# Optimization experiments

Hardware: AMD Instinct MI355X
Metric: run time of the kernel (lower is better)

## Reference

```python
import jax, jax.numpy as jnp
import numpy as np

B, N, NFEAT, NHID, NOUT, NMLP, NCLASS = 32, 1024, 128, 64, 64, 128, 2
ALPHA = 0.2  # leaky relu slope
NEG = -9e15


def setup_inputs() -> dict:
    key = jax.random.key(0)
    ks = jax.random.split(key, 12)
    x = jax.random.normal(ks[0], (B, N, NFEAT), dtype=jnp.float32)
    x_mask = (jax.random.uniform(ks[1], (B, N)) < 0.9).astype(jnp.float32)
    adj = (jax.random.uniform(ks[2], (B, N, N)) < 0.05).astype(jnp.float32)
    adj = jnp.maximum(adj, jnp.eye(N, dtype=jnp.float32)[None])  # self loops
    s = 0.02
    W0 = jax.random.normal(ks[3], (NFEAT, NHID), dtype=jnp.float32) * s
    a0 = jax.random.normal(ks[4], (2 * NHID, 1), dtype=jnp.float32) * s
    Wout = jax.random.normal(ks[5], (NHID, NOUT), dtype=jnp.float32) * s
    aout = jax.random.normal(ks[6], (2 * NOUT, 1), dtype=jnp.float32) * s
    W1 = jax.random.normal(ks[7], (NOUT, NMLP), dtype=jnp.float32) * s
    b1 = jnp.zeros((NMLP,), dtype=jnp.float32)
    W2 = jax.random.normal(ks[8], (NMLP, NCLASS), dtype=jnp.float32) * s
    b2 = jnp.zeros((NCLASS,), dtype=jnp.float32)
    return {"x": x, "x_mask": x_mask, "adj": adj, "W0": W0, "a0": a0,
            "Wout": Wout, "aout": aout, "W1": W1, "b1": b1, "W2": W2, "b2": b2}


def _gat_layer(h, adj, W, a):
    # h: [B,N,F_in], W: [F_in,F_out], a: [2*F_out,1]
    Wh = jnp.einsum('bnf,fh->bnh', h, W)                 # [B,N,F_out]
    d = W.shape[1]
    f1 = Wh @ a[:d]                                      # [B,N,1]
    f2 = Wh @ a[d:]                                      # [B,N,1]
    e = jax.nn.leaky_relu(f1 + jnp.swapaxes(f2, 1, 2), ALPHA)  # [B,N,N]
    e = jnp.where(adj > 0, e, NEG)
    attn = jax.nn.softmax(e, axis=-1)
    return jnp.einsum('bnm,bmh->bnh', attn, Wh)


def reference(x, x_mask, adj, W0, a0, Wout, aout, W1, b1, W2, b2):
    # Only head 0 reaches out_att in the original (zip truncation); dropout is
    # identity in eval mode.
    h = jax.nn.elu(_gat_layer(x, adj, W0, a0))           # concat=True -> elu
    h = jax.nn.elu(_gat_layer(h, adj, Wout, aout))       # F.elu applied outside
    m = x_mask[..., None]
    g = jnp.sum(h * m, axis=1) / jnp.maximum(jnp.sum(x_mask, axis=1, keepdims=True), 1.0)  # masked mean readout [B,NOUT]
    return jax.nn.relu(g @ W1 + b1) @ W2 + b2            # [B,NCLASS]
```

## Files before the change

kernel.cpp:

```cpp
#include <hip/hip_runtime.h>
#include <math.h>

#define BB 32
#define NN 1024
#define NFEAT 128
#define ALPHA 0.2f
#define MAXD 128

#define WH1_TILE_BLOCKS (BB * NN / 64)
#define ATTN_BLOCKS (BB * NN / 4)

template<int FIN>
__device__ __forceinline__ void wh_tile_body(
    const int blk, const int tid,
    const float* __restrict__ hin, const float* __restrict__ W,
    const float* __restrict__ a, float* __restrict__ Wh,
    float* __restrict__ f1, float* __restrict__ f2) {
  const int tx = tid & 15;
  const int ty = tid >> 4;
  const int row0 = blk * 64 + ty * 4;

  float4 acc[4];
#pragma unroll
  for (int i = 0; i < 4; ++i) acc[i] = make_float4(0.f, 0.f, 0.f, 0.f);

#pragma unroll 4
  for (int k = 0; k < FIN; k += 4) {
    float4 wv[4];
#pragma unroll
    for (int i = 0; i < 4; ++i)
      wv[i] = *reinterpret_cast<const float4*>(&W[(size_t)(k + i) * 64 + tx * 4]);
#pragma unroll
    for (int i = 0; i < 4; ++i) {
      const float4 xv = *reinterpret_cast<const float4*>(
          &hin[(size_t)(row0 + i) * FIN + k]);
      acc[i].x = fmaf(xv.x, wv[0].x, acc[i].x);
      acc[i].y = fmaf(xv.x, wv[0].y, acc[i].y);
      acc[i].z = fmaf(xv.x, wv[0].z, acc[i].z);
      acc[i].w = fmaf(xv.x, wv[0].w, acc[i].w);
      acc[i].x = fmaf(xv.y, wv[1].x, acc[i].x);
      acc[i].y = fmaf(xv.y, wv[1].y, acc[i].y);
      acc[i].z = fmaf(xv.y, wv[1].z, acc[i].z);
      acc[i].w = fmaf(xv.y, wv[1].w, acc[i].w);
      acc[i].x = fmaf(xv.z, wv[2].x, acc[i].x);
      acc[i].y = fmaf(xv.z, wv[2].y, acc[i].y);
      acc[i].z = fmaf(xv.z, wv[2].z, acc[i].z);
      acc[i].w = fmaf(xv.z, wv[2].w, acc[i].w);
      acc[i].x = fmaf(xv.w, wv[3].x, acc[i].x);
      acc[i].y = fmaf(xv.w, wv[3].y, acc[i].y);
      acc[i].z = fmaf(xv.w, wv[3].z, acc[i].z);
      acc[i].w = fmaf(xv.w, wv[3].w, acc[i].w);
    }
  }

  const float4 av1 = *reinterpret_cast<const float4*>(&a[tx * 4]);
  const float4 av2 = *reinterpret_cast<const float4*>(&a[64 + tx * 4]);
#pragma unroll
  for (int i = 0; i < 4; ++i) {
    const int row = row0 + i;
    *reinterpret_cast<float4*>(&Wh[(size_t)row * 64 + tx * 4]) = acc[i];
    float c1 = acc[i].x * av1.x + acc[i].y * av1.y + acc[i].z * av1.z + acc[i].w * av1.w;
    float c2 = acc[i].x * av2.x + acc[i].y * av2.y + acc[i].z * av2.z + acc[i].w * av2.w;
#pragma unroll
    for (int off = 8; off > 0; off >>= 1) {
      c1 += __shfl_xor(c1, off, 64);
      c2 += __shfl_xor(c2, off, 64);
    }
    if (tx == 0) { f1[row] = c1; f2[row] = c2; }
  }
}

__global__ __launch_bounds__(256) void wh1_kernel(
    const float* __restrict__ x, const float* __restrict__ W0,
    const float* __restrict__ a0, float* __restrict__ Wh,
    float* __restrict__ f1, float* __restrict__ f2) {
  wh_tile_body<NFEAT>(blockIdx.x, threadIdx.x, x, W0, a0, Wh, f1, f2);
}

__global__ __launch_bounds__(256) void nbr_build_kernel(
    const float* __restrict__ adj, unsigned short* __restrict__ nbr,
    int* __restrict__ cnt) {
  __shared__ unsigned short stageW[4][128];
  __shared__ unsigned short merged[MAXD];
  __shared__ int cnts[4];
  const int row = blockIdx.x;
  const int wv = threadIdx.x >> 6, lane = threadIdx.x & 63;
  const float* adjrow = adj + (size_t)row * NN;

  const float4 av = *reinterpret_cast<const float4*>(&adjrow[wv * 256 + lane * 4]);
  if (threadIdx.x < 64)
    reinterpret_cast<unsigned int*>(merged)[threadIdx.x] = 0u;

  const unsigned long long lmask = (1ull << lane) - 1ull;
  const int m = (av.x > 0.f ? 1 : 0) | (av.y > 0.f ? 2 : 0) |
                (av.z > 0.f ? 4 : 0) | (av.w > 0.f ? 8 : 0);
  const unsigned long long b0 = __ballot(m & 1);
  const unsigned long long b1 = __ballot(m & 2);
  const unsigned long long b2 = __ballot(m & 4);
  const unsigned long long b3 = __ballot(m & 8);
  int base = __popcll(b0 & lmask) + __popcll(b1 & lmask) +
             __popcll(b2 & lmask) + __popcll(b3 & lmask);
  const int e0 = wv * 256 + lane * 4;
  if (m & 1) { if (base < 128) stageW[wv][base] = (unsigned short)(e0);     ++base; }
  if (m & 2) { if (base < 128) stageW[wv][base] = (unsigned short)(e0 + 1); ++base; }
  if (m & 4) { if (base < 128) stageW[wv][base] = (unsigned short)(e0 + 2); ++base; }
  if (m & 8) { if (base < 128) stageW[wv][base] = (unsigned short)(e0 + 3); ++base; }
  if (lane == 0)
    cnts[wv] = __popcll(b0) + __popcll(b1) + __popcll(b2) + __popcll(b3);
  __syncthreads();
  const int c0 = cnts[0], c1 = cnts[1], c2 = cnts[2], c3 = cnts[3];
  const int off = (wv == 0) ? 0 : (wv == 1) ? c0 : (wv == 2) ? c0 + c1 : c0 + c1 + c2;
  const int cw  = (wv == 0) ? c0 : (wv == 1) ? c1 : (wv == 2) ? c2 : c3;
  if (lane < cw && off + lane < MAXD) merged[off + lane] = stageW[wv][lane];
  if (64 + lane < cw && off + 64 + lane < MAXD)
    merged[off + 64 + lane] = stageW[wv][64 + lane];
  __syncthreads();
  if (threadIdx.x < 64)
    reinterpret_cast<unsigned int*>(nbr + (size_t)row * MAXD)[threadIdx.x] =
        reinterpret_cast<const unsigned int*>(merged)[threadIdx.x];
  if (threadIdx.x == 0) {
    const int total = c0 + c1 + c2 + c3;
    cnt[row] = total < MAXD ? total : MAXD;
  }
}

__device__ __forceinline__ void attn_softmax(
    const unsigned short* __restrict__ nrow, const int count,
    const float f1n, const float* __restrict__ f2b,
    float* ps, unsigned short* msh, const int lane) {
  int m0 = 0, m1 = 0;
  const bool on0 = lane < count, on1 = 64 + lane < count;
  float e0 = -3e38f, e1 = -3e38f;
  if (on0) { m0 = nrow[lane];      float v = f1n + f2b[m0]; e0 = v > 0.f ? v : ALPHA * v; }
  if (on1) { m1 = nrow[64 + lane]; float v = f1n + f2b[m1]; e1 = v > 0.f ? v : ALPHA * v; }
  float lmax = fmaxf(e0, e1);
#pragma unroll
  for (int off = 32; off > 0; off >>= 1) lmax = fmaxf(lmax, __shfl_xor(lmax, off, 64));
  float p0 = on0 ? __expf(e0 - lmax) : 0.f;
  float p1 = on1 ? __expf(e1 - lmax) : 0.f;
  float ls = p0 + p1;
#pragma unroll
  for (int off = 32; off > 0; off >>= 1) ls += __shfl_xor(ls, off, 64);
  const float inv = 1.f / ls;
  ps[lane] = p0 * inv;  ps[64 + lane] = p1 * inv;
  msh[lane] = (unsigned short)m0;  msh[64 + lane] = (unsigned short)m1;
}

__device__ __forceinline__ float attn_gather(
    const float* ps, const unsigned short* msh, const int count,
    const float* __restrict__ Whb, const int lane) {
  float a0 = 0.f, a1 = 0.f, a2 = 0.f, a3 = 0.f;
  float a4 = 0.f, a5 = 0.f, a6 = 0.f, a7 = 0.f;
  const int c8 = count & ~7;
  int k = 0;
  for (; k < c8; k += 8) {
    const float4  pa = *reinterpret_cast<const float4*>(&ps[k]);
    const float4  pb = *reinterpret_cast<const float4*>(&ps[k + 4]);
    const ushort4 ia = *reinterpret_cast<const ushort4*>(&msh[k]);
    const ushort4 ib = *reinterpret_cast<const ushort4*>(&msh[k + 4]);
    a0 = fmaf(pa.x, Whb[(size_t)ia.x * 64 + lane], a0);
    a1 = fmaf(pa.y, Whb[(size_t)ia.y * 64 + lane], a1);
    a2 = fmaf(pa.z, Whb[(size_t)ia.z * 64 + lane], a2);
    a3 = fmaf(pa.w, Whb[(size_t)ia.w * 64 + lane], a3);
    a4 = fmaf(pb.x, Whb[(size_t)ib.x * 64 + lane], a4);
    a5 = fmaf(pb.y, Whb[(size_t)ib.y * 64 + lane], a5);
    a6 = fmaf(pb.z, Whb[(size_t)ib.z * 64 + lane], a6);
    a7 = fmaf(pb.w, Whb[(size_t)ib.w * 64 + lane], a7);
  }
  for (; k < count; ++k)
    a0 = fmaf(ps[k], Whb[(size_t)msh[k] * 64 + lane], a0);
  return ((a0 + a1) + (a2 + a3)) + ((a4 + a5) + (a6 + a7));
}

__global__ __launch_bounds__(256) void attn1_kernel(
    const unsigned short* __restrict__ nbr, const int* __restrict__ cnt,
    const float* __restrict__ f1, const float* __restrict__ f2,
    const float* __restrict__ Wh,
    const float* __restrict__ Wnext, const float* __restrict__ anext,
    float* __restrict__ WhOut, float* __restrict__ f1o,
    float* __restrict__ f2o) {
  __shared__ float ps[4][MAXD];
  __shared__ unsigned short msh[4][MAXD];
  __shared__ float h1s[4][64];
  const int wv = threadIdx.x >> 6, lane = threadIdx.x & 63;
  const int j = blockIdx.x;
  const int batch = (j & 7) + 8 * (j >> 11);
  const int chunk = (j >> 3) & 255;
  const int row = (batch * 256 + chunk) * 4 + wv;

  int count = cnt[row];
  if (count > MAXD) count = MAXD;
  attn_softmax(nbr + (size_t)row * MAXD, count, f1[row],
               f2 + (size_t)batch * NN, ps[wv], msh[wv], lane);
  const float acc = attn_gather(ps[wv], msh[wv], count,
                                Wh + (size_t)batch * (NN * 64), lane);
  const float hval = acc > 0.f ? acc : expm1f(acc);

  h1s[wv][lane] = hval;
  float s = 0.f;
#pragma unroll 8
  for (int f = 0; f < 64; ++f)
    s = fmaf(h1s[wv][f], Wnext[f * 64 + lane], s);
  WhOut[(size_t)row * 64 + lane] = s;
  float c1 = s * anext[lane];
  float c2 = s * anext[64 + lane];
#pragma unroll
  for (int off = 32; off > 0; off >>= 1) {
    c1 += __shfl_xor(c1, off, 64);
    c2 += __shfl_xor(c2, off, 64);
  }
  if (lane == 0) { f1o[row] = c1; f2o[row] = c2; }
}

__global__ __launch_bounds__(256) void attn2_kernel(
    const unsigned short* __restrict__ nbr, const int* __restrict__ cnt,
    const float* __restrict__ f1, const float* __restrict__ f2,
    const float* __restrict__ Wh, const float* __restrict__ mask,
    float* __restrict__ part2) {
  __shared__ float ps[4][MAXD];
  __shared__ unsigned short msh[4][MAXD];
  __shared__ float agg[4][64];
  const int wv = threadIdx.x >> 6, lane = threadIdx.x & 63;
  const int j = blockIdx.x;
  const int batch = (j & 7) + 8 * (j >> 11);
  const int chunk = (j >> 3) & 255;
  const int row = (batch * 256 + chunk) * 4 + wv;

  int count = cnt[row];
  if (count > MAXD) count = MAXD;
  attn_softmax(nbr + (size_t)row * MAXD, count, f1[row],
               f2 + (size_t)batch * NN, ps[wv], msh[wv], lane);
  const float acc = attn_gather(ps[wv], msh[wv], count,
                                Wh + (size_t)batch * (NN * 64), lane);
  const float hval = acc > 0.f ? acc : expm1f(acc);

  const float mv = mask[row];
  agg[wv][lane] = mv * hval;
  __syncthreads();
  if (wv == 0)
    part2[(size_t)(batch * 256 + chunk) * 64 + lane] =
        (agg[0][lane] + agg[1][lane]) + (agg[2][lane] + agg[3][lane]);
}

__global__ __launch_bounds__(256) void mlp2_kernel(
    const float* __restrict__ part2, const float* __restrict__ mask,
    const float* __restrict__ W1, const float* __restrict__ b1,
    const float* __restrict__ W2, const float* __restrict__ b2,
    float* __restrict__ outp) {
  const int b = blockIdx.x;
  const int tid = threadIdx.x;
  const int wv = tid >> 6, lane = tid & 63;
  __shared__ float aggG[4][64];
  __shared__ float msW[4];
  __shared__ float g[64];
  __shared__ float hid[128];

  const float4 mv4 = *reinterpret_cast<const float4*>(&mask[(size_t)b * NN + tid * 4]);
  float ms = (mv4.x + mv4.y) + (mv4.z + mv4.w);
#pragma unroll
  for (int off = 32; off > 0; off >>= 1) ms += __shfl_xor(ms, off, 64);
  if (lane == 0) msW[wv] = ms;

  float gs = 0.f;
  const float* pb = part2 + ((size_t)b * 256 + wv * 64) * 64 + lane;
#pragma unroll 8
  for (int i = 0; i < 64; ++i) gs += pb[(size_t)i * 64];
  aggG[wv][lane] = gs;
  __syncthreads();
  const float denom = fmaxf((msW[0] + msW[1]) + (msW[2] + msW[3]), 1.0f);
  if (tid < 64)
    g[tid] = ((aggG[0][tid] + aggG[1][tid]) + (aggG[2][tid] + aggG[3][tid])) / denom;
  __syncthreads();
  if (tid < 128) {
    float s = b1[tid];
#pragma unroll 8
    for (int k = 0; k < 64; ++k) s += g[k] * W1[k * 128 + tid];
    hid[tid] = fmaxf(s, 0.f);
  }
  __syncthreads();
  if (tid < 2) {
    float o = b2[tid];
    for (int jj = 0; jj < 128; ++jj) o += hid[jj] * W2[jj * 2 + tid];
    outp[b * 2 + tid] = o;
  }
}

extern "C" void kernel_launch(void* const* d_in, const int* in_sizes, int n_in,
                              void* d_out, int out_size, void* d_ws, size_t ws_size,
                              hipStream_t stream) {
  const float* x      = (const float*)d_in[0];
  const float* x_mask = (const float*)d_in[1];
  const float* adj    = (const float*)d_in[2];
  const float* W0     = (const float*)d_in[3];
  const float* a0     = (const float*)d_in[4];
  const float* Wout   = (const float*)d_in[5];
  const float* aout   = (const float*)d_in[6];
  const float* W1     = (const float*)d_in[7];
  const float* b1     = (const float*)d_in[8];
  const float* W2     = (const float*)d_in[9];
  const float* b2     = (const float*)d_in[10];
  float* out = (float*)d_out;

  const int rows = BB * NN;

  float* ws = (float*)d_ws;
  float* Wh  = ws;
  float* Wh2 = Wh + (size_t)rows * 64;
  float* f1  = Wh2 + (size_t)rows * 64;
  float* f2  = f1 + rows;
  float* f1b = f2 + rows;
  float* f2b = f1b + rows;
  int*   cnt = (int*)(f2b + rows);
  unsigned short* nbr = (unsigned short*)(cnt + rows);
  float* part2 = (float*)(nbr + (size_t)rows * MAXD);

  nbr_build_kernel<<<rows, 256, 0, stream>>>(adj, nbr, cnt);
  wh1_kernel<<<WH1_TILE_BLOCKS, 256, 0, stream>>>(x, W0, a0, Wh, f1, f2);
  attn1_kernel<<<ATTN_BLOCKS, 256, 0, stream>>>(
      nbr, cnt, f1, f2, Wh, Wout, aout, Wh2, f1b, f2b);
  attn2_kernel<<<ATTN_BLOCKS, 256, 0, stream>>>(
      nbr, cnt, f1b, f2b, Wh2, x_mask, part2);
  mlp2_kernel<<<BB, 256, 0, stream>>>(part2, x_mask, W1, b1, W2, b2, out);
}
```

Measured before the change: 119.3 us.

## Fuse adjacency neighbor-list build into first attention kernel

Removes the separate neighbor-list construction kernel and instead has each wavefront in the first attention kernel scan its own adjacency row, compact the neighbor indices into shared memory via ballot/popcount, and write the list and count out for the second attention layer. This saves a kernel launch and the separate global write-then-read of the neighbor list in layer 1. In exchange, each wave now serially scans a 1024-wide row (4 float4 loads per lane) before the softmax, so the adj read is spread across a kernel with different occupancy.

```diff
diff --git a/kernel.cpp b/kernel.cpp
--- a/kernel.cpp
+++ b/kernel.cpp
@@ -77,75 +77,6 @@
   wh_tile_body<NFEAT>(blockIdx.x, threadIdx.x, x, W0, a0, Wh, f1, f2);
 }
 
-__global__ __launch_bounds__(256) void nbr_build_kernel(
-    const float* __restrict__ adj, unsigned short* __restrict__ nbr,
-    int* __restrict__ cnt) {
-  __shared__ unsigned short stageW[4][128];
-  __shared__ unsigned short merged[MAXD];
-  __shared__ int cnts[4];
-  const int row = blockIdx.x;
-  const int wv = threadIdx.x >> 6, lane = threadIdx.x & 63;
-  const float* adjrow = adj + (size_t)row * NN;
-
-  const float4 av = *reinterpret_cast<const float4*>(&adjrow[wv * 256 + lane * 4]);
-  if (threadIdx.x < 64)
-    reinterpret_cast<unsigned int*>(merged)[threadIdx.x] = 0u;
-
-  const unsigned long long lmask = (1ull << lane) - 1ull;
-  const int m = (av.x > 0.f ? 1 : 0) | (av.y > 0.f ? 2 : 0) |
-                (av.z > 0.f ? 4 : 0) | (av.w > 0.f ? 8 : 0);
-  const unsigned long long b0 = __ballot(m & 1);
-  const unsigned long long b1 = __ballot(m & 2);
-  const unsigned long long b2 = __ballot(m & 4);
-  const unsigned long long b3 = __ballot(m & 8);
-  int base = __popcll(b0 & lmask) + __popcll(b1 & lmask) +
-             __popcll(b2 & lmask) + __popcll(b3 & lmask);
-  const int e0 = wv * 256 + lane * 4;
-  if (m & 1) { if (base < 128) stageW[wv][base] = (unsigned short)(e0);     ++base; }
-  if (m & 2) { if (base < 128) stageW[wv][base] = (unsigned short)(e0 + 1); ++base; }
-  if (m & 4) { if (base < 128) stageW[wv][base] = (unsigned short)(e0 + 2); ++base; }
-  if (m & 8) { if (base < 128) stageW[wv][base] = (unsigned short)(e0 + 3); ++base; }
-  if (lane == 0)
-    cnts[wv] = __popcll(b0) + __popcll(b1) + __popcll(b2) + __popcll(b3);
-  __syncthreads();
-  const int c0 = cnts[0], c1 = cnts[1], c2 = cnts[2], c3 = cnts[3];
-  const int off = (wv == 0) ? 0 : (wv == 1) ? c0 : (wv == 2) ? c0 + c1 : c0 + c1 + c2;
-  const int cw  = (wv == 0) ? c0 : (wv == 1) ? c1 : (wv == 2) ? c2 : c3;
-  if (lane < cw && off + lane < MAXD) merged[off + lane] = stageW[wv][lane];
-  if (64 + lane < cw && off + 64 + lane < MAXD)
-    merged[off + 64 + lane] = stageW[wv][64 + lane];
-  __syncthreads();
-  if (threadIdx.x < 64)
-    reinterpret_cast<unsigned int*>(nbr + (size_t)row * MAXD)[threadIdx.x] =
-        reinterpret_cast<const unsigned int*>(merged)[threadIdx.x];
-  if (threadIdx.x == 0) {
-    const int total = c0 + c1 + c2 + c3;
-    cnt[row] = total < MAXD ? total : MAXD;
-  }
-}
-
-__device__ __forceinline__ void attn_softmax(
-    const unsigned short* __restrict__ nrow, const int count,
-    const float f1n, const float* __restrict__ f2b,
-    float* ps, unsigned short* msh, const int lane) {
-  int m0 = 0, m1 = 0;
-  const bool on0 = lane < count, on1 = 64 + lane < count;
-  float e0 = -3e38f, e1 = -3e38f;
-  if (on0) { m0 = nrow[lane];      float v = f1n + f2b[m0]; e0 = v > 0.f ? v : ALPHA * v; }
-  if (on1) { m1 = nrow[64 + lane]; float v = f1n + f2b[m1]; e1 = v > 0.f ? v : ALPHA * v; }
-  float lmax = fmaxf(e0, e1);
-#pragma unroll
-  for (int off = 32; off > 0; off >>= 1) lmax = fmaxf(lmax, __shfl_xor(lmax, off, 64));
-  float p0 = on0 ? __expf(e0 - lmax) : 0.f;
-  float p1 = on1 ? __expf(e1 - lmax) : 0.f;
-  float ls = p0 + p1;
-#pragma unroll
-  for (int off = 32; off > 0; off >>= 1) ls += __shfl_xor(ls, off, 64);
-  const float inv = 1.f / ls;
-  ps[lane] = p0 * inv;  ps[64 + lane] = p1 * inv;
-  msh[lane] = (unsigned short)m0;  msh[64 + lane] = (unsigned short)m1;
-}
-
 __device__ __forceinline__ float attn_gather(
     const float* ps, const unsigned short* msh, const int count,
     const float* __restrict__ Whb, const int lane) {
@@ -172,11 +103,12 @@
   return ((a0 + a1) + (a2 + a3)) + ((a4 + a5) + (a6 + a7));
 }
 
-__global__ __launch_bounds__(256) void attn1_kernel(
-    const unsigned short* __restrict__ nbr, const int* __restrict__ cnt,
+__global__ __launch_bounds__(256) void scan_attn1_kernel(
+    const float* __restrict__ adj,
     const float* __restrict__ f1, const float* __restrict__ f2,
     const float* __restrict__ Wh,
     const float* __restrict__ Wnext, const float* __restrict__ anext,
+    unsigned short* __restrict__ nbr, int* __restrict__ cnt,
     float* __restrict__ WhOut, float* __restrict__ f1o,
     float* __restrict__ f2o) {
   __shared__ float ps[4][MAXD];
@@ -188,10 +120,59 @@
   const int chunk = (j >> 3) & 255;
   const int row = (batch * 256 + chunk) * 4 + wv;
 
-  int count = cnt[row];
+  const float* adjrow = adj + (size_t)row * NN;
+  float4 av[4];
+#pragma unroll
+  for (int c = 0; c < 4; ++c)
+    av[c] = *reinterpret_cast<const float4*>(&adjrow[c * 256 + lane * 4]);
+  msh[wv][lane] = 0;
+  msh[wv][64 + lane] = 0;
+  const unsigned long long lmask = (1ull << lane) - 1ull;
+  int count = 0;
+#pragma unroll
+  for (int c = 0; c < 4; ++c) {
+    const int m = (av[c].x > 0.f ? 1 : 0) | (av[c].y > 0.f ? 2 : 0) |
+                  (av[c].z > 0.f ? 4 : 0) | (av[c].w > 0.f ? 8 : 0);
+    const unsigned long long b0 = __ballot(m & 1);
+    const unsigned long long b1 = __ballot(m & 2);
+    const unsigned long long b2 = __ballot(m & 4);
+    const unsigned long long b3 = __ballot(m & 8);
+    int base = count + __popcll(b0 & lmask) + __popcll(b1 & lmask) +
+               __popcll(b2 & lmask) + __popcll(b3 & lmask);
+    const int e0 = c * 256 + lane * 4;
+    if (m & 1) { if (base < MAXD) msh[wv][base] = (unsigned short)(e0);     ++base; }
+    if (m & 2) { if (base < MAXD) msh[wv][base] = (unsigned short)(e0 + 1); ++base; }
+    if (m & 4) { if (base < MAXD) msh[wv][base] = (unsigned short)(e0 + 2); ++base; }
+    if (m & 8) { if (base < MAXD) msh[wv][base] = (unsigned short)(e0 + 3); ++base; }
+    count += __popcll(b0) + __popcll(b1) + __popcll(b2) + __popcll(b3);
+  }
   if (count > MAXD) count = MAXD;
-  attn_softmax(nbr + (size_t)row * MAXD, count, f1[row],
-               f2 + (size_t)batch * NN, ps[wv], msh[wv], lane);
+  if (lane == 0) cnt[row] = count;
+  {
+    const unsigned int lo = msh[wv][2 * lane];
+    const unsigned int hi = msh[wv][2 * lane + 1];
+    reinterpret_cast<unsigned int*>(nbr + (size_t)row * MAXD)[lane] =
+        lo | (hi << 16);
+  }
+
+  const float f1n = f1[row];
+  const float* f2b = f2 + (size_t)batch * NN;
+  int m0 = 0, m1 = 0;
+  const bool on0 = lane < count, on1 = 64 + lane < count;
+  float e0v = -3e38f, e1v = -3e38f;
+  if (on0) { m0 = msh[wv][lane];      float v = f1n + f2b[m0]; e0v = v > 0.f ? v : ALPHA * v; }
+  if (on1) { m1 = msh[wv][64 + lane]; float v = f1n + f2b[m1]; e1v = v > 0.f ? v : ALPHA * v; }
+  float lmax = fmaxf(e0v, e1v);
+#pragma unroll
+  for (int off = 32; off > 0; off >>= 1) lmax = fmaxf(lmax, __shfl_xor(lmax, off, 64));
+  float p0 = on0 ? __expf(e0v - lmax) : 0.f;
+  float p1 = on1 ? __expf(e1v - lmax) : 0.f;
+  float ls = p0 + p1;
+#pragma unroll
+  for (int off = 32; off > 0; off >>= 1) ls += __shfl_xor(ls, off, 64);
+  const float inv = 1.f / ls;
+  ps[wv][lane] = p0 * inv;  ps[wv][64 + lane] = p1 * inv;
+
   const float acc = attn_gather(ps[wv], msh[wv], count,
                                 Wh + (size_t)batch * (NN * 64), lane);
   const float hval = acc > 0.f ? acc : expm1f(acc);
@@ -228,8 +209,26 @@
 
   int count = cnt[row];
   if (count > MAXD) count = MAXD;
-  attn_softmax(nbr + (size_t)row * MAXD, count, f1[row],
-               f2 + (size_t)batch * NN, ps[wv], msh[wv], lane);
+  const unsigned short* nrow = nbr + (size_t)row * MAXD;
+  const float f1n = f1[row];
+  const float* f2b = f2 + (size_t)batch * NN;
+  int m0 = 0, m1 = 0;
+  const bool on0 = lane < count, on1 = 64 + lane < count;
+  float e0v = -3e38f, e1v = -3e38f;
+  if (on0) { m0 = nrow[lane];      float v = f1n + f2b[m0]; e0v = v > 0.f ? v : ALPHA * v; }
+  if (on1) { m1 = nrow[64 + lane]; float v = f1n + f2b[m1]; e1v = v > 0.f ? v : ALPHA * v; }
+  float lmax = fmaxf(e0v, e1v);
+#pragma unroll
+  for (int off = 32; off > 0; off >>= 1) lmax = fmaxf(lmax, __shfl_xor(lmax, off, 64));
+  float p0 = on0 ? __expf(e0v - lmax) : 0.f;
+  float p1 = on1 ? __expf(e1v - lmax) : 0.f;
+  float ls = p0 + p1;
+#pragma unroll
+  for (int off = 32; off > 0; off >>= 1) ls += __shfl_xor(ls, off, 64);
+  const float inv = 1.f / ls;
+  ps[wv][lane] = p0 * inv;  ps[wv][64 + lane] = p1 * inv;
+  msh[wv][lane] = (unsigned short)m0;  msh[wv][64 + lane] = (unsigned short)m1;
+
   const float acc = attn_gather(ps[wv], msh[wv], count,
                                 Wh + (size_t)batch * (NN * 64), lane);
   const float hval = acc > 0.f ? acc : expm1f(acc);
@@ -314,10 +313,9 @@
   unsigned short* nbr = (unsigned short*)(cnt + rows);
   float* part2 = (float*)(nbr + (size_t)rows * MAXD);
 
-  nbr_build_kernel<<<rows, 256, 0, stream>>>(adj, nbr, cnt);
   wh1_kernel<<<WH1_TILE_BLOCKS, 256, 0, stream>>>(x, W0, a0, Wh, f1, f2);
-  attn1_kernel<<<ATTN_BLOCKS, 256, 0, stream>>>(
-      nbr, cnt, f1, f2, Wh, Wout, aout, Wh2, f1b, f2b);
+  scan_attn1_kernel<<<ATTN_BLOCKS, 256, 0, stream>>>(
+      adj, f1, f2, Wh, Wout, aout, nbr, cnt, Wh2, f1b, f2b);
   attn2_kernel<<<ATTN_BLOCKS, 256, 0, stream>>>(
       nbr, cnt, f1b, f2b, Wh2, x_mask, part2);
   mlp2_kernel<<<BB, 256, 0, stream>>>(part2, x_mask, W1, b1, W2, b2, out);
```

After: 106.5 us. 1.12x faster.
